# Performance work log

Measured on AMD Instinct MI355X. Metric: run time of the kernel, lower is better.

Reference implementation:

```python
import jax, jax.numpy as jnp
import numpy as np

N, E = 50000, 800000
IN_DIM, OUT_DIM, H = 256, 128, 8
GEO_HID = 16  # RBF feature dim and geo_mlp hidden dim


def setup_inputs() -> dict:
    key = jax.random.key(0)
    ks = jax.random.split(key, 16)
    def lin(k, fan_out, fan_in):
        kw, kb = jax.random.split(k)
        lim = 1.0 / np.sqrt(fan_in)
        W = jax.random.uniform(kw, (fan_out, fan_in), jnp.float32, -lim, lim)
        b = jax.random.uniform(kb, (fan_out,), jnp.float32, -lim, lim)
        return W, b
    Wq, bq = lin(ks[0], OUT_DIM, IN_DIM)
    Wk, bk = lin(ks[1], OUT_DIM, IN_DIM)
    Wv, bv = lin(ks[2], OUT_DIM, IN_DIM)
    Wo, bo = lin(ks[3], OUT_DIM, OUT_DIM)
    Wg1, bg1 = lin(ks[4], GEO_HID, GEO_HID)
    Wg2, bg2 = lin(ks[5], H, GEO_HID)
    x = jax.random.normal(ks[6], (N, IN_DIM), jnp.float32)
    edge_index = jax.random.randint(ks[7], (2, E), 0, N, jnp.int64)
    edge_dist = jax.random.uniform(ks[8], (E,), jnp.float32) * 6.0
    return {"x": x, "edge_index": edge_index, "edge_dist": edge_dist,
            "Wq": Wq, "bq": bq, "Wk": Wk, "bk": bk, "Wv": Wv, "bv": bv,
            "Wo": Wo, "bo": bo, "Wg1": Wg1, "bg1": bg1, "Wg2": Wg2, "bg2": bg2}


def reference(x, edge_index, edge_dist, Wq, bq, Wk, bk, Wv, bv, Wo, bo, Wg1, bg1, Wg2, bg2):
    n = x.shape[0]
    num_heads = Wg2.shape[0]
    head_dim = Wq.shape[0] // num_heads
    scale = 1.0 / (head_dim ** 0.5)

    q = (x @ Wq.T + bq).reshape(n, num_heads, head_dim)
    k = (x @ Wk.T + bk).reshape(n, num_heads, head_dim)
    v = (x @ Wv.T + bv).reshape(n, num_heads, head_dim)

    # RBF expansion: 16 centers in [0, 6], gamma = 1.0
    centers = jnp.linspace(0.0, 6.0, GEO_HID)
    rbf = jnp.exp(-(edge_dist[:, None] - centers) ** 2)          # [E, 16]
    geo_bias = jax.nn.relu(rbf @ Wg1.T + bg1) @ Wg2.T + bg2      # [E, H]

    row, col = edge_index[0], edge_index[1]
    attn = (q[row] * k[col]).sum(-1) * scale + geo_bias          # [E, H]

    # segment softmax over incoming edges per destination node (row)
    m = jax.ops.segment_max(attn, row, num_segments=n)           # [N, H]
    e = jnp.exp(attn - m[row])
    s = jax.ops.segment_sum(e, row, num_segments=n)              # [N, H]
    a = e / (s[row] + 1e-12)                                     # [E, H]

    out = jax.ops.segment_sum(v[col] * a[:, :, None], row, num_segments=n)
    out = out.reshape(n, num_heads * head_dim)
    return out @ Wo.T + bo
```

## Files before the change

### kernel.cpp

```cpp
#include <hip/hip_runtime.h>
#include <math.h>

#define IN_DIM 256
#define OUT_DIM 128
#define NH 8
#define HD 16
#define GH 16
#define TBL 1024
#define LOG2E 1.44269504f
#define DPAD 32
#define RCAP 64

typedef __attribute__((ext_vector_type(8))) short short8;
typedef __attribute__((ext_vector_type(4))) float floatx4;

__device__ __forceinline__ unsigned short f2bf(float f) {
    union { float f; unsigned u; } v; v.f = f;
    unsigned r = v.u + 0x7fffu + ((v.u >> 16) & 1u);
    return (unsigned short)(r >> 16);
}
__device__ __forceinline__ float bf2f(unsigned short h) {
    union { unsigned u; float f; } v; v.u = ((unsigned)h) << 16;
    return v.f;
}
__device__ __forceinline__ void split1(float f, unsigned short& h, unsigned short& l) {
    h = f2bf(f);
    l = f2bf(f - bf2f(h));
}
__device__ __forceinline__ float bflo(unsigned u) { return __uint_as_float(u << 16); }
__device__ __forceinline__ float bfhi(unsigned u) { return __uint_as_float(u & 0xffff0000u); }

__global__ __launch_bounds__(256) void prep_all_kernel(
    const float* __restrict__ x, const float* __restrict__ Wq, const float* __restrict__ Wk,
    const float* __restrict__ Wv, const float* __restrict__ Wo,
    unsigned short* __restrict__ xh, unsigned short* __restrict__ xl,
    unsigned short* __restrict__ wh, unsigned short* __restrict__ wl,
    unsigned short* __restrict__ wo_h, unsigned short* __restrict__ wo_l,
    const float* __restrict__ Wg1, const float* __restrict__ bg1,
    const float* __restrict__ Wg2, const float* __restrict__ bg2,
    float* __restrict__ tbl, int* __restrict__ cnt,
    int n4x, int Nzero, int nsplit, int nwm, int nwo, int ngeo, int ndegz) {
    int bx = blockIdx.x;
    int t = threadIdx.x;

    if (bx < nsplit) {
        int i = bx * 256 + t;
        if (i >= n4x) return;
        float4 f = ((const float4*)x)[i];
        ushort4 h, l;
        split1(f.x, h.x, l.x); split1(f.y, h.y, l.y);
        split1(f.z, h.z, l.z); split1(f.w, h.w, l.w);
        ((ushort4*)xh)[i] = h;
        ((ushort4*)xl)[i] = l;
        return;
    }
    bx -= nsplit;
    if (bx < 3 * nwm) {
        int m = bx / nwm;
        int i = (bx - m * nwm) * 256 + t;
        if (i >= (OUT_DIM * IN_DIM) / 4) return;
        const float* W = (m == 0) ? Wq : (m == 1) ? Wk : Wv;
        float4 f = ((const float4*)W)[i];
        ushort4 h, l;
        split1(f.x, h.x, l.x); split1(f.y, h.y, l.y);
        split1(f.z, h.z, l.z); split1(f.w, h.w, l.w);
        size_t base = (size_t)m * (OUT_DIM * IN_DIM) / 4;
        ((ushort4*)wh)[base + i] = h;
        ((ushort4*)wl)[base + i] = l;
        return;
    }
    bx -= 3 * nwm;
    if (bx < nwo) {
        int i = bx * 256 + t;
        if (i >= (OUT_DIM * OUT_DIM) / 4) return;
        float4 f = ((const float4*)Wo)[i];
        ushort4 h, l;
        split1(f.x, h.x, l.x); split1(f.y, h.y, l.y);
        split1(f.z, h.z, l.z); split1(f.w, h.w, l.w);
        ((ushort4*)wo_h)[i] = h;
        ((ushort4*)wo_l)[i] = l;
        return;
    }
    bx -= nwo;
    if (bx < ngeo) {
        int i = bx * 256 + t;
        if (i >= TBL) return;
        float d = (float)i * (6.0f / (float)(TBL - 1));
        float rbf[GH];
#pragma unroll
        for (int j = 0; j < GH; ++j) {
            float c = 0.4f * (float)j;
            float tt = d - c;
            rbf[j] = __expf(-tt * tt);
        }
        float hid[GH];
#pragma unroll
        for (int j = 0; j < GH; ++j) {
            float acc = bg1[j];
#pragma unroll
            for (int kk = 0; kk < GH; ++kk) acc += rbf[kk] * Wg1[j * GH + kk];
            hid[j] = fmaxf(acc, 0.0f);
        }
#pragma unroll
        for (int h = 0; h < NH; ++h) {
            float acc = bg2[h];
#pragma unroll
            for (int j = 0; j < GH; ++j) acc += hid[j] * Wg2[h * GH + j];
            tbl[i * NH + h] = acc * LOG2E;
        }
        return;
    }
    bx -= ngeo;
    if (bx < ndegz) {
        int idx4 = (bx * 256 + t) * 4;
        if (idx4 + 3 < Nzero) {
            *(int4*)(cnt + idx4) = make_int4(0, 0, 0, 0);
        } else {
#pragma unroll
            for (int j = 0; j < 4; ++j) if (idx4 + j < Nzero) cnt[idx4 + j] = 0;
        }
        return;
    }
}

__device__ __forceinline__ void scatter_body(int i0, int stride, const int* __restrict__ ei,
                                             const float* __restrict__ edist, int* __restrict__ cnt,
                                             int2* __restrict__ bucket, int E_) {
    for (int e = i0; e < E_; e += stride) {
        int row = ei[e];
        int pos = atomicAdd(&cnt[row * DPAD], 1);
        float u = edist[e] * ((float)(TBL - 1) / 6.0f);
        u = fminf(fmaxf(u, 0.0f), (float)(TBL - 1));
        if (pos < RCAP) bucket[(size_t)row * RCAP + pos] = make_int2(ei[E_ + e], __float_as_int(u));
    }
}

__global__ __launch_bounds__(256) void qkv_kernel(
    const unsigned short* __restrict__ xh, const unsigned short* __restrict__ xl,
    const unsigned short* __restrict__ wh, const unsigned short* __restrict__ wl,
    const float* __restrict__ bq, const float* __restrict__ bk, const float* __restrict__ bv,
    float* __restrict__ q, unsigned short* __restrict__ kb, unsigned short* __restrict__ vb,
    const int* __restrict__ ei, const float* __restrict__ edist,
    int* __restrict__ cnt, int2* __restrict__ bucket,
    int Nn, int E_, int nxb) {
    int bx = blockIdx.x;
    if (bx >= 3 * nxb) {
        int nb = gridDim.x - 3 * nxb;
        int i0 = (bx - 3 * nxb) * 256 + threadIdx.x;
        scatter_body(i0, nb * 256, ei, edist, cnt, bucket, E_);
        return;
    }
    const int wsel = bx / nxb;
    const int n0 = (bx - wsel * nxb) * 128;
    const unsigned short* W_h = wh + (size_t)wsel * (OUT_DIM * IN_DIM);
    const unsigned short* W_l = wl + (size_t)wsel * (OUT_DIM * IN_DIM);
    const float* bias = (wsel == 0) ? bq : (wsel == 1) ? bk : bv;
    const bool vpath = (wsel == 2);

    __shared__ unsigned short xh_s[128 * 40];
    __shared__ unsigned short xl_s[128 * 40];
    __shared__ unsigned short wh_s[128 * 40];
    __shared__ unsigned short wl_s[128 * 40];

    const int tid = threadIdx.x;
    const int w = tid >> 6;
    const int lane = tid & 63;
    const int ml = lane & 15;
    const int quad = lane >> 4;

    const int rows_valid = min(128, Nn - n0);

    floatx4 acc[2][8];
#pragma unroll
    for (int rr = 0; rr < 2; ++rr)
#pragma unroll
        for (int ct = 0; ct < 8; ++ct) acc[rr][ct] = (floatx4){0.f, 0.f, 0.f, 0.f};

    const short8 zero8 = {0, 0, 0, 0, 0, 0, 0, 0};

    for (int kc = 0; kc < IN_DIM; kc += 32) {
#pragma unroll
        for (int l = 0; l < 2; ++l) {
            int flat = tid + l * 256;
            int r = flat >> 2, c = flat & 3;
            size_t gx = (size_t)(n0 + r) * IN_DIM + kc + c * 8;
            size_t gw = (size_t)r * IN_DIM + kc + c * 8;
            short8 vh = zero8;
            if (r < rows_valid) vh = *(const short8*)(xh + gx);
            *(short8*)(xh_s + r * 40 + c * 8) = vh;
            *(short8*)(wh_s + r * 40 + c * 8) = *(const short8*)(W_h + gw);
            if (vpath) {
                short8 vl = zero8;
                if (r < rows_valid) vl = *(const short8*)(xl + gx);
                *(short8*)(xl_s + r * 40 + c * 8) = vl;
                *(short8*)(wl_s + r * 40 + c * 8) = *(const short8*)(W_l + gw);
            }
        }
        __syncthreads();

        short8 ah0 = *(const short8*)(xh_s + (w * 32 + ml) * 40 + quad * 8);
        short8 ah1 = *(const short8*)(xh_s + (w * 32 + 16 + ml) * 40 + quad * 8);
        if (!vpath) {
#pragma unroll
            for (int ct = 0; ct < 8; ++ct) {
                short8 bh = *(const short8*)(wh_s + (ct * 16 + ml) * 40 + quad * 8);
                acc[0][ct] = __builtin_amdgcn_mfma_f32_16x16x32_bf16(ah0, bh, acc[0][ct], 0, 0, 0);
                acc[1][ct] = __builtin_amdgcn_mfma_f32_16x16x32_bf16(ah1, bh, acc[1][ct], 0, 0, 0);
            }
        } else {
            short8 al0 = *(const short8*)(xl_s + (w * 32 + ml) * 40 + quad * 8);
            short8 al1 = *(const short8*)(xl_s + (w * 32 + 16 + ml) * 40 + quad * 8);
#pragma unroll
            for (int ct = 0; ct < 8; ++ct) {
                short8 bh = *(const short8*)(wh_s + (ct * 16 + ml) * 40 + quad * 8);
                short8 bl = *(const short8*)(wl_s + (ct * 16 + ml) * 40 + quad * 8);
                acc[0][ct] = __builtin_amdgcn_mfma_f32_16x16x32_bf16(ah0, bh, acc[0][ct], 0, 0, 0);
                acc[0][ct] = __builtin_amdgcn_mfma_f32_16x16x32_bf16(al0, bh, acc[0][ct], 0, 0, 0);
                acc[0][ct] = __builtin_amdgcn_mfma_f32_16x16x32_bf16(ah0, bl, acc[0][ct], 0, 0, 0);
                acc[1][ct] = __builtin_amdgcn_mfma_f32_16x16x32_bf16(ah1, bh, acc[1][ct], 0, 0, 0);
                acc[1][ct] = __builtin_amdgcn_mfma_f32_16x16x32_bf16(al1, bh, acc[1][ct], 0, 0, 0);
                acc[1][ct] = __builtin_amdgcn_mfma_f32_16x16x32_bf16(ah1, bl, acc[1][ct], 0, 0, 0);
            }
        }
        __syncthreads();
    }

    if (wsel == 0) {
#pragma unroll
        for (int rr = 0; rr < 2; ++rr)
#pragma unroll
            for (int ct = 0; ct < 8; ++ct) {
                float bj = bias[ct * 16 + ml];
#pragma unroll
                for (int r = 0; r < 4; ++r) {
                    int grow = n0 + w * 32 + rr * 16 + quad * 4 + r;
                    if (grow < Nn) q[(size_t)grow * 128 + ct * 16 + ml] = acc[rr][ct][r] + bj;
                }
            }
    } else {
        unsigned short* ob = (wsel == 1) ? kb : vb;
#pragma unroll
        for (int rr = 0; rr < 2; ++rr)
#pragma unroll
            for (int ct = 0; ct < 8; ++ct) {
                float bj = bias[ct * 16 + ml];
#pragma unroll
                for (int r = 0; r < 4; ++r) {
                    int grow = n0 + w * 32 + rr * 16 + quad * 4 + r;
                    if (grow < Nn) ob[(size_t)grow * 128 + ct * 16 + ml] = f2bf(acc[rr][ct][r] + bj);
                }
            }
    }
}

__global__ __launch_bounds__(256) void scatter_kernel(const int* __restrict__ ei, const float* __restrict__ edist,
                                                      int* __restrict__ cnt, int2* __restrict__ bucket, int E_) {
    int i0 = blockIdx.x * 256 + threadIdx.x;
    scatter_body(i0, gridDim.x * 256, ei, edist, cnt, bucket, E_);
}

__global__ __launch_bounds__(256) void fused_node_kernel(
    const float* __restrict__ q, const unsigned short* __restrict__ kb,
    const unsigned short* __restrict__ vb, const int2* __restrict__ bucket,
    const float* __restrict__ tbl, const int* __restrict__ cnt,
    unsigned short* __restrict__ oh, unsigned short* __restrict__ ol, int Nn) {
    int lane = threadIdx.x & 63;
    int n = blockIdx.x * 4 + (threadIdx.x >> 6);
    if (n >= Nn) return;
    int g = lane >> 3;
    int h = lane & 7;
    int dcnt = cnt[n * DPAD];
    if (dcnt > RCAP) dcnt = RCAP;
    int start = n * RCAP;
    int end = start + dcnt;

    float qf[16];
    {
        const float4* qp = (const float4*)(q + (size_t)n * 128 + h * 16);
#pragma unroll
        for (int j = 0; j < 4; ++j) {
            float4 t = qp[j];
            qf[j * 4 + 0] = t.x; qf[j * 4 + 1] = t.y;
            qf[j * 4 + 2] = t.z; qf[j * 4 + 3] = t.w;
        }
    }

    float l = 0.0f;
    float acc[16];
#pragma unroll
    for (int j = 0; j < 16; ++j) acc[j] = 0.0f;

#pragma unroll 2
    for (int base = start; base < end; base += 8) {
        int e = base + g;
        bool valid = (e < end);
        int ee = valid ? e : (end - 1);
        int2 np = bucket[ee];
        int col = np.x;
        float u = __int_as_float(np.y);

        const uint4* kp = (const uint4*)(kb + (size_t)col * 128 + h * 16);
        uint4 k0 = kp[0], k1 = kp[1];
        const uint4* vp = (const uint4*)(vb + (size_t)col * 128 + h * 16);
        uint4 v0 = vp[0], v1 = vp[1];

        unsigned kk[8] = {k0.x, k0.y, k0.z, k0.w, k1.x, k1.y, k1.z, k1.w};
        float d = 0.0f;
#pragma unroll
        for (int j = 0; j < 8; ++j) {
            d = fmaf(bflo(kk[j]), qf[2 * j], d);
            d = fmaf(bfhi(kk[j]), qf[2 * j + 1], d);
        }

        int i0 = min((int)u, TBL - 2);
        float fr = u - (float)i0;
        float t0 = tbl[i0 * NH + h];
        float t1 = tbl[i0 * NH + NH + h];
        float logit2 = fmaf(d, 0.25f * LOG2E, fmaf(fr, t1 - t0, t0));
        logit2 = fminf(logit2, 80.0f);
        if (!valid) logit2 = -1e30f;
        float p = __builtin_amdgcn_exp2f(logit2);

        l += p;
        unsigned vv[8] = {v0.x, v0.y, v0.z, v0.w, v1.x, v1.y, v1.z, v1.w};
#pragma unroll
        for (int j = 0; j < 8; ++j) {
            acc[2 * j]     = fmaf(p, bflo(vv[j]), acc[2 * j]);
            acc[2 * j + 1] = fmaf(p, bfhi(vv[j]), acc[2 * j + 1]);
        }
    }

#pragma unroll
    for (int off = 8; off < 64; off <<= 1) {
        l += __shfl_xor(l, off);
#pragma unroll
        for (int j = 0; j < 16; ++j) acc[j] += __shfl_xor(acc[j], off);
    }

    if (g == 0) {
        float inv = 1.0f / (l + 1e-12f);
        unsigned short hv[16], lv[16];
#pragma unroll
        for (int j = 0; j < 16; ++j) {
            float o = acc[j] * inv;
            split1(o, hv[j], lv[j]);
        }
        *(short8*)(oh + (size_t)n * 128 + h * 16) = *(short8*)hv;
        *(short8*)(oh + (size_t)n * 128 + h * 16 + 8) = *(short8*)(hv + 8);
        *(short8*)(ol + (size_t)n * 128 + h * 16) = *(short8*)lv;
        *(short8*)(ol + (size_t)n * 128 + h * 16 + 8) = *(short8*)(lv + 8);
    }
}

__global__ __launch_bounds__(256) void out_gemm_mfma_kernel(
    const unsigned short* __restrict__ oh, const unsigned short* __restrict__ ol,
    const unsigned short* __restrict__ wo_h, const unsigned short* __restrict__ wo_l,
    const float* __restrict__ bo, float* __restrict__ out, int Nn) {
    const int n0 = blockIdx.x * 64;

    __shared__ unsigned short xh_s[64 * 40];
    __shared__ unsigned short xl_s[64 * 40];
    __shared__ unsigned short wh_s[128 * 40];
    __shared__ unsigned short wl_s[128 * 40];

    const int tid = threadIdx.x;
    const int w = tid >> 6;
    const int lane = tid & 63;
    const int ml = lane & 15;
    const int quad = lane >> 4;

    const int rows_valid = min(64, Nn - n0);

    floatx4 acc[8];
#pragma unroll
    for (int ct = 0; ct < 8; ++ct) acc[ct] = (floatx4){0.f, 0.f, 0.f, 0.f};

    const short8 zero8 = {0, 0, 0, 0, 0, 0, 0, 0};

    for (int kc = 0; kc < OUT_DIM; kc += 32) {
        {
            int r = tid >> 2, c = tid & 3;
            short8 vh = zero8, vl = zero8;
            if (r < rows_valid) {
                size_t g = (size_t)(n0 + r) * OUT_DIM + kc + c * 8;
                vh = *(const short8*)(oh + g);
                vl = *(const short8*)(ol + g);
            }
            *(short8*)(xh_s + r * 40 + c * 8) = vh;
            *(short8*)(xl_s + r * 40 + c * 8) = vl;
        }
#pragma unroll
        for (int l = 0; l < 2; ++l) {
            int idx = tid + l * 256;
            int r = idx >> 2, c = idx & 3;
            size_t g = (size_t)r * OUT_DIM + kc + c * 8;
            *(short8*)(wh_s + r * 40 + c * 8) = *(const short8*)(wo_h + g);
            *(short8*)(wl_s + r * 40 + c * 8) = *(const short8*)(wo_l + g);
        }
        __syncthreads();

        short8 ah = *(const short8*)(xh_s + (w * 16 + ml) * 40 + quad * 8);
        short8 al = *(const short8*)(xl_s + (w * 16 + ml) * 40 + quad * 8);
#pragma unroll
        for (int ct = 0; ct < 8; ++ct) {
            short8 bh = *(const short8*)(wh_s + (ct * 16 + ml) * 40 + quad * 8);
            short8 bl = *(const short8*)(wl_s + (ct * 16 + ml) * 40 + quad * 8);
            acc[ct] = __builtin_amdgcn_mfma_f32_16x16x32_bf16(ah, bh, acc[ct], 0, 0, 0);
            acc[ct] = __builtin_amdgcn_mfma_f32_16x16x32_bf16(al, bh, acc[ct], 0, 0, 0);
            acc[ct] = __builtin_amdgcn_mfma_f32_16x16x32_bf16(ah, bl, acc[ct], 0, 0, 0);
        }
        __syncthreads();
    }

#pragma unroll
    for (int ct = 0; ct < 8; ++ct) {
        float bj = bo[ct * 16 + ml];
#pragma unroll
        for (int r = 0; r < 4; ++r) {
            int grow = n0 + w * 16 + quad * 4 + r;
            if (grow < Nn) out[(size_t)grow * 128 + ct * 16 + ml] = acc[ct][r] + bj;
        }
    }
}

extern "C" void kernel_launch(void* const* d_in, const int* in_sizes, int n_in,
                              void* d_out, int out_size, void* d_ws, size_t ws_size,
                              hipStream_t stream) {
    const float* x   = (const float*)d_in[0];
    const int* ei    = (const int*)d_in[1];
    const float* edist = (const float*)d_in[2];
    const float* Wq = (const float*)d_in[3];  const float* bq = (const float*)d_in[4];
    const float* Wk = (const float*)d_in[5];  const float* bk = (const float*)d_in[6];
    const float* Wv = (const float*)d_in[7];  const float* bv = (const float*)d_in[8];
    const float* Wo = (const float*)d_in[9];  const float* bo = (const float*)d_in[10];
    const float* Wg1 = (const float*)d_in[11]; const float* bg1 = (const float*)d_in[12];
    const float* Wg2 = (const float*)d_in[13]; const float* bg2 = (const float*)d_in[14];
    const int Nn = in_sizes[0] / IN_DIM;
    const int Ee = in_sizes[2];
    float* out = (float*)d_out;

    char* ws = (char*)d_ws;
    size_t off = 0;
    auto alloc = [&](size_t bytes) -> char* {
        char* p = ws + off;
        off += (bytes + 255) & ~(size_t)255;
        return p;
    };
    float* q  = (float*)alloc((size_t)Nn * 128 * 4);
    unsigned short* kbuf = (unsigned short*)alloc((size_t)Nn * 128 * 2);
    unsigned short* vbuf = (unsigned short*)alloc((size_t)Nn * 128 * 2);
    char* xlblock = alloc((size_t)Nn * IN_DIM * 2);
    unsigned short* o_hi = (unsigned short*)alloc((size_t)Nn * 128 * 2);
    unsigned short* o_lo = (unsigned short*)alloc((size_t)Nn * 128 * 2);
    float* geot = (float*)alloc((size_t)TBL * 8 * 4);
    int* cnt      = (int*)alloc((size_t)Nn * DPAD * 4);
    unsigned short* wh_all = (unsigned short*)alloc((size_t)3 * OUT_DIM * IN_DIM * 2);
    unsigned short* wl_all = (unsigned short*)alloc((size_t)3 * OUT_DIM * IN_DIM * 2);
    unsigned short* wo_h = (unsigned short*)alloc((size_t)OUT_DIM * OUT_DIM * 2);
    unsigned short* wo_l = (unsigned short*)alloc((size_t)OUT_DIM * OUT_DIM * 2);
    int2* bucket_sep = (int2*)alloc((size_t)Nn * RCAP * 8);

    const bool fuse_scat = (off <= ws_size);
    int2* bucket = fuse_scat ? bucket_sep : (int2*)xlblock;

    unsigned short* xh = (unsigned short*)d_out;
    unsigned short* xl = (unsigned short*)xlblock;

    int n4x = Nn * IN_DIM / 4;
    int nsplit = (n4x + 255) / 256;
    int nwm = ((OUT_DIM * IN_DIM / 4) + 255) / 256;
    int nwo = ((OUT_DIM * OUT_DIM / 4) + 255) / 256;
    int ngeo = (TBL + 255) / 256;
    int Nzero = Nn * DPAD;
    int ndegz = (Nzero + 1023) / 1024;
    int gprep = nsplit + 3 * nwm + nwo + ngeo + ndegz;
    prep_all_kernel<<<gprep, 256, 0, stream>>>(
        x, Wq, Wk, Wv, Wo, xh, xl, wh_all, wl_all, wo_h, wo_l,
        Wg1, bg1, Wg2, bg2, geot, cnt, n4x, Nzero, nsplit, nwm, nwo, ngeo, ndegz);

    int nxb = (Nn + 127) / 128;
    if (fuse_scat) {
        qkv_kernel<<<3 * nxb + 2048, 256, 0, stream>>>(
            xh, xl, wh_all, wl_all, bq, bk, bv, q, kbuf, vbuf,
            ei, edist, cnt, bucket, Nn, Ee, nxb);
    } else {
        qkv_kernel<<<3 * nxb, 256, 0, stream>>>(
            xh, xl, wh_all, wl_all, bq, bk, bv, q, kbuf, vbuf,
            ei, edist, cnt, bucket, Nn, Ee, nxb);
        scatter_kernel<<<1024, 256, 0, stream>>>(ei, edist, cnt, bucket, Ee);
    }

    fused_node_kernel<<<(Nn + 3) / 4, 256, 0, stream>>>(q, kbuf, vbuf, bucket, geot, cnt, o_hi, o_lo, Nn);

    out_gemm_mfma_kernel<<<(Nn + 63) / 64, 256, 0, stream>>>(o_hi, o_lo, wo_h, wo_l, bo, out, Nn);
}
```

Baseline: 299.5 us.

## Replace global-atomic edge scatter with two-pass binned bucketing via LDS histograms

Edges are first grouped into 128-node bins: per-block LDS histograms reserve ranges with one global atomic per bin, and packed (col,rowrel,dist) records go into a bin buffer. A new bin2bucket kernel then distributes each bin into per-row buckets using LDS atomics and writes compact counts. This removes per-edge global atomics and the large padded count array with its zeroing pass. The attention output is also stored as fp32 and split into bf16 hi/lo inside the output GEMM, and the bin buffer reuses the output buffer; this adds a kernel launch and has a fixed per-bin capacity.

```diff
diff --git a/kernel.cpp b/kernel.cpp
--- a/kernel.cpp
+++ b/kernel.cpp
@@ -8,8 +8,8 @@
 #define GH 16
 #define TBL 1024
 #define LOG2E 1.44269504f
-#define DPAD 32
 #define RCAP 64
+#define BCAP 2560
 
 typedef __attribute__((ext_vector_type(8))) short short8;
 typedef __attribute__((ext_vector_type(4))) float floatx4;
@@ -38,8 +38,8 @@
     unsigned short* __restrict__ wo_h, unsigned short* __restrict__ wo_l,
     const float* __restrict__ Wg1, const float* __restrict__ bg1,
     const float* __restrict__ Wg2, const float* __restrict__ bg2,
-    float* __restrict__ tbl, int* __restrict__ cnt,
-    int n4x, int Nzero, int nsplit, int nwm, int nwo, int ngeo, int ndegz) {
+    float* __restrict__ tbl, int* __restrict__ gbin,
+    int n4x, int nbins, int nsplit, int nwm, int nwo, int ngeo) {
     int bx = blockIdx.x;
     int t = threadIdx.x;
 
@@ -110,29 +110,7 @@
         }
         return;
     }
-    bx -= ngeo;
-    if (bx < ndegz) {
-        int idx4 = (bx * 256 + t) * 4;
-        if (idx4 + 3 < Nzero) {
-            *(int4*)(cnt + idx4) = make_int4(0, 0, 0, 0);
-        } else {
-#pragma unroll
-            for (int j = 0; j < 4; ++j) if (idx4 + j < Nzero) cnt[idx4 + j] = 0;
-        }
-        return;
-    }
-}
-
-__device__ __forceinline__ void scatter_body(int i0, int stride, const int* __restrict__ ei,
-                                             const float* __restrict__ edist, int* __restrict__ cnt,
-                                             int2* __restrict__ bucket, int E_) {
-    for (int e = i0; e < E_; e += stride) {
-        int row = ei[e];
-        int pos = atomicAdd(&cnt[row * DPAD], 1);
-        float u = edist[e] * ((float)(TBL - 1) / 6.0f);
-        u = fminf(fmaxf(u, 0.0f), (float)(TBL - 1));
-        if (pos < RCAP) bucket[(size_t)row * RCAP + pos] = make_int2(ei[E_ + e], __float_as_int(u));
-    }
+    for (int i = t; i < nbins; i += 256) gbin[i] = 0;
 }
 
 __global__ __launch_bounds__(256) void qkv_kernel(
@@ -141,15 +119,52 @@
     const float* __restrict__ bq, const float* __restrict__ bk, const float* __restrict__ bv,
     float* __restrict__ q, unsigned short* __restrict__ kb, unsigned short* __restrict__ vb,
     const int* __restrict__ ei, const float* __restrict__ edist,
-    int* __restrict__ cnt, int2* __restrict__ bucket,
-    int Nn, int E_, int nxb) {
+    int* __restrict__ gbin, int2* __restrict__ binbuf,
+    int Nn, int E_, int nxb, int nb1, int nbins) {
+    __shared__ unsigned short xh_s[128 * 40];
+    __shared__ unsigned short xl_s[128 * 40];
+    __shared__ unsigned short wh_s[128 * 40];
+    __shared__ unsigned short wl_s[128 * 40];
+
+    const int tid = threadIdx.x;
     int bx = blockIdx.x;
-    if (bx >= 3 * nxb) {
-        int nb = gridDim.x - 3 * nxb;
-        int i0 = (bx - 3 * nxb) * 256 + threadIdx.x;
-        scatter_body(i0, nb * 256, ei, edist, cnt, bucket, E_);
+
+    if (bx < nb1) {
+        int* hist = (int*)xh_s;
+        const int e0 = bx * 4096;
+        for (int b = tid; b < nbins; b += 256) hist[b] = 0;
+        __syncthreads();
+#pragma unroll
+        for (int i = 0; i < 16; ++i) {
+            int e = e0 + tid + i * 256;
+            if (e < E_) atomicAdd(&hist[ei[e] >> 7], 1);
+        }
+        __syncthreads();
+        for (int b = tid; b < nbins; b += 256) {
+            int h = hist[b];
+            int base = 0;
+            if (h) base = atomicAdd(&gbin[b], h);
+            hist[b] = base;
+        }
+        __syncthreads();
+#pragma unroll
+        for (int i = 0; i < 16; ++i) {
+            int e = e0 + tid + i * 256;
+            if (e < E_) {
+                int row = ei[e];
+                int bin = row >> 7;
+                int r = atomicAdd(&hist[bin], 1);
+                float u = edist[e] * ((float)(TBL - 1) / 6.0f);
+                u = fminf(fmaxf(u, 0.0f), (float)(TBL - 1));
+                if (r < BCAP)
+                    binbuf[(size_t)bin * BCAP + r] =
+                        make_int2((ei[E_ + e] & 0x1FFFF) | ((row & 127) << 17), __float_as_int(u));
+            }
+        }
         return;
     }
+    bx -= nb1;
+
     const int wsel = bx / nxb;
     const int n0 = (bx - wsel * nxb) * 128;
     const unsigned short* W_h = wh + (size_t)wsel * (OUT_DIM * IN_DIM);
@@ -157,12 +172,6 @@
     const float* bias = (wsel == 0) ? bq : (wsel == 1) ? bk : bv;
     const bool vpath = (wsel == 2);
 
-    __shared__ unsigned short xh_s[128 * 40];
-    __shared__ unsigned short xl_s[128 * 40];
-    __shared__ unsigned short wh_s[128 * 40];
-    __shared__ unsigned short wl_s[128 * 40];
-
-    const int tid = threadIdx.x;
     const int w = tid >> 6;
     const int lane = tid & 63;
     const int ml = lane & 15;
@@ -253,24 +262,39 @@
     }
 }
 
-__global__ __launch_bounds__(256) void scatter_kernel(const int* __restrict__ ei, const float* __restrict__ edist,
-                                                      int* __restrict__ cnt, int2* __restrict__ bucket, int E_) {
-    int i0 = blockIdx.x * 256 + threadIdx.x;
-    scatter_body(i0, gridDim.x * 256, ei, edist, cnt, bucket, E_);
+__global__ __launch_bounds__(256) void bin2bucket_kernel(
+    const int2* __restrict__ binbuf, const int* __restrict__ gbin,
+    int2* __restrict__ bucket, int* __restrict__ cnt, int Nn) {
+    __shared__ int rcnt[128];
+    const int bin = blockIdx.x;
+    const int t = threadIdx.x;
+    if (t < 128) rcnt[t] = 0;
+    __syncthreads();
+    int nb = gbin[bin];
+    if (nb > BCAP) nb = BCAP;
+    const int row0 = bin << 7;
+    for (int i = t; i < nb; i += 256) {
+        int2 p = binbuf[(size_t)bin * BCAP + i];
+        int rowrel = (p.x >> 17) & 127;
+        int col = p.x & 0x1FFFF;
+        int r = atomicAdd(&rcnt[rowrel], 1);
+        if (r < RCAP) bucket[(size_t)(row0 + rowrel) * RCAP + r] = make_int2(col, p.y);
+    }
+    __syncthreads();
+    if (t < 128 && row0 + t < Nn) cnt[row0 + t] = min(rcnt[t], RCAP);
 }
 
 __global__ __launch_bounds__(256) void fused_node_kernel(
     const float* __restrict__ q, const unsigned short* __restrict__ kb,
     const unsigned short* __restrict__ vb, const int2* __restrict__ bucket,
     const float* __restrict__ tbl, const int* __restrict__ cnt,
-    unsigned short* __restrict__ oh, unsigned short* __restrict__ ol, int Nn) {
+    float* __restrict__ o, int Nn) {
     int lane = threadIdx.x & 63;
     int n = blockIdx.x * 4 + (threadIdx.x >> 6);
     if (n >= Nn) return;
     int g = lane >> 3;
     int h = lane & 7;
-    int dcnt = cnt[n * DPAD];
-    if (dcnt > RCAP) dcnt = RCAP;
+    int dcnt = cnt[n];
     int start = n * RCAP;
     int end = start + dcnt;
 
@@ -339,21 +363,19 @@
 
     if (g == 0) {
         float inv = 1.0f / (l + 1e-12f);
-        unsigned short hv[16], lv[16];
-#pragma unroll
-        for (int j = 0; j < 16; ++j) {
-            float o = acc[j] * inv;
-            split1(o, hv[j], lv[j]);
-        }
-        *(short8*)(oh + (size_t)n * 128 + h * 16) = *(short8*)hv;
-        *(short8*)(oh + (size_t)n * 128 + h * 16 + 8) = *(short8*)(hv + 8);
-        *(short8*)(ol + (size_t)n * 128 + h * 16) = *(short8*)lv;
-        *(short8*)(ol + (size_t)n * 128 + h * 16 + 8) = *(short8*)(lv + 8);
+        float4* op = (float4*)(o + (size_t)n * 128 + h * 16);
+#pragma unroll
+        for (int j = 0; j < 4; ++j) {
+            float4 t;
+            t.x = acc[j * 4 + 0] * inv; t.y = acc[j * 4 + 1] * inv;
+            t.z = acc[j * 4 + 2] * inv; t.w = acc[j * 4 + 3] * inv;
+            op[j] = t;
+        }
     }
 }
 
 __global__ __launch_bounds__(256) void out_gemm_mfma_kernel(
-    const unsigned short* __restrict__ oh, const unsigned short* __restrict__ ol,
+    const float* __restrict__ o,
     const unsigned short* __restrict__ wo_h, const unsigned short* __restrict__ wo_l,
     const float* __restrict__ bo, float* __restrict__ out, int Nn) {
     const int n0 = blockIdx.x * 64;
@@ -375,19 +397,20 @@
 #pragma unroll
     for (int ct = 0; ct < 8; ++ct) acc[ct] = (floatx4){0.f, 0.f, 0.f, 0.f};
 
-    const short8 zero8 = {0, 0, 0, 0, 0, 0, 0, 0};
-
     for (int kc = 0; kc < OUT_DIM; kc += 32) {
         {
             int r = tid >> 2, c = tid & 3;
-            short8 vh = zero8, vl = zero8;
+            unsigned short hv[8], lv[8];
             if (r < rows_valid) {
-                size_t g = (size_t)(n0 + r) * OUT_DIM + kc + c * 8;
-                vh = *(const short8*)(oh + g);
-                vl = *(const short8*)(ol + g);
-            }
-            *(short8*)(xh_s + r * 40 + c * 8) = vh;
-            *(short8*)(xl_s + r * 40 + c * 8) = vl;
+                const float* src = o + (size_t)(n0 + r) * OUT_DIM + kc + c * 8;
+#pragma unroll
+                for (int j = 0; j < 8; ++j) split1(src[j], hv[j], lv[j]);
+            } else {
+#pragma unroll
+                for (int j = 0; j < 8; ++j) { hv[j] = 0; lv[j] = 0; }
+            }
+            *(short8*)(xh_s + r * 40 + c * 8) = *(short8*)hv;
+            *(short8*)(xl_s + r * 40 + c * 8) = *(short8*)lv;
         }
 #pragma unroll
         for (int l = 0; l < 2; ++l) {
@@ -450,18 +473,18 @@
     unsigned short* kbuf = (unsigned short*)alloc((size_t)Nn * 128 * 2);
     unsigned short* vbuf = (unsigned short*)alloc((size_t)Nn * 128 * 2);
     char* xlblock = alloc((size_t)Nn * IN_DIM * 2);
-    unsigned short* o_hi = (unsigned short*)alloc((size_t)Nn * 128 * 2);
-    unsigned short* o_lo = (unsigned short*)alloc((size_t)Nn * 128 * 2);
+    float* o = (float*)alloc((size_t)Nn * 128 * 4);
     float* geot = (float*)alloc((size_t)TBL * 8 * 4);
-    int* cnt      = (int*)alloc((size_t)Nn * DPAD * 4);
+    int* cnt = (int*)alloc((size_t)Nn * 4);
+    int nbins = (Nn + 127) >> 7;
+    int* gbin = (int*)alloc((size_t)nbins * 4);
     unsigned short* wh_all = (unsigned short*)alloc((size_t)3 * OUT_DIM * IN_DIM * 2);
     unsigned short* wl_all = (unsigned short*)alloc((size_t)3 * OUT_DIM * IN_DIM * 2);
     unsigned short* wo_h = (unsigned short*)alloc((size_t)OUT_DIM * OUT_DIM * 2);
     unsigned short* wo_l = (unsigned short*)alloc((size_t)OUT_DIM * OUT_DIM * 2);
-    int2* bucket_sep = (int2*)alloc((size_t)Nn * RCAP * 8);
-
-    const bool fuse_scat = (off <= ws_size);
-    int2* bucket = fuse_scat ? bucket_sep : (int2*)xlblock;
+    int2* bucket = (int2*)alloc((size_t)Nn * RCAP * 8);
+
+    int2* binbuf = (int2*)o;
 
     unsigned short* xh = (unsigned short*)d_out;
     unsigned short* xl = (unsigned short*)xlblock;
@@ -471,26 +494,20 @@
     int nwm = ((OUT_DIM * IN_DIM / 4) + 255) / 256;
     int nwo = ((OUT_DIM * OUT_DIM / 4) + 255) / 256;
     int ngeo = (TBL + 255) / 256;
-    int Nzero = Nn * DPAD;
-    int ndegz = (Nzero + 1023) / 1024;
-    int gprep = nsplit + 3 * nwm + nwo + ngeo + ndegz;
+    int gprep = nsplit + 3 * nwm + nwo + ngeo + 1;
     prep_all_kernel<<<gprep, 256, 0, stream>>>(
         x, Wq, Wk, Wv, Wo, xh, xl, wh_all, wl_all, wo_h, wo_l,
-        Wg1, bg1, Wg2, bg2, geot, cnt, n4x, Nzero, nsplit, nwm, nwo, ngeo, ndegz);
+        Wg1, bg1, Wg2, bg2, geot, gbin, n4x, nbins, nsplit, nwm, nwo, ngeo);
 
     int nxb = (Nn + 127) / 128;
-    if (fuse_scat) {
-        qkv_kernel<<<3 * nxb + 2048, 256, 0, stream>>>(
-            xh, xl, wh_all, wl_all, bq, bk, bv, q, kbuf, vbuf,
-            ei, edist, cnt, bucket, Nn, Ee, nxb);
-    } else {
-        qkv_kernel<<<3 * nxb, 256, 0, stream>>>(
-            xh, xl, wh_all, wl_all, bq, bk, bv, q, kbuf, vbuf,
-            ei, edist, cnt, bucket, Nn, Ee, nxb);
-        scatter_kernel<<<1024, 256, 0, stream>>>(ei, edist, cnt, bucket, Ee);
-    }
-
-    fused_node_kernel<<<(Nn + 3) / 4, 256, 0, stream>>>(q, kbuf, vbuf, bucket, geot, cnt, o_hi, o_lo, Nn);
-
-    out_gemm_mfma_kernel<<<(Nn + 63) / 64, 256, 0, stream>>>(o_hi, o_lo, wo_h, wo_l, bo, out, Nn);
-}
+    int nb1 = (Ee + 4095) / 4096;
+    qkv_kernel<<<nb1 + 3 * nxb, 256, 0, stream>>>(
+        xh, xl, wh_all, wl_all, bq, bk, bv, q, kbuf, vbuf,
+        ei, edist, gbin, binbuf, Nn, Ee, nxb, nb1, nbins);
+
+    bin2bucket_kernel<<<nbins, 256, 0, stream>>>(binbuf, gbin, bucket, cnt, Nn);
+
+    fused_node_kernel<<<(Nn + 3) / 4, 256, 0, stream>>>(q, kbuf, vbuf, bucket, geot, cnt, o, Nn);
+
+    out_gemm_mfma_kernel<<<(Nn + 63) / 64, 256, 0, stream>>>(o, wo_h, wo_l, bo, out, Nn);
+}
```

Result: faster. 289.3 us (-3.4%).
